# Kernel optimization log

Measured on AMD Instinct MI355X. Metric: run time of the kernel, lower is better.

The kernel has to match this reference:

```python
import jax, jax.numpy as jnp
import numpy as np

N = 10000      # nodes
E = 160000     # edges (before self-loops)
IN = 128       # input channels
H1, C1 = 8, 128   # layer-1 heads / per-head channels
OUT = 64       # output channels
NEG_SLOPE = 0.2   # PyG GATConv leaky_relu slope


def _glorot(key, shape):
    fan = shape[0] + shape[-1]
    return jax.random.normal(key, shape, jnp.float32) * np.float32(np.sqrt(2.0 / fan))


def setup_inputs() -> dict:
    key = jax.random.key(0)
    ks = jax.random.split(key, 10)
    x = jax.random.normal(ks[0], (N, IN), jnp.float32)
    edge_index = jax.random.randint(ks[1], (2, E), 0, N, dtype=jnp.int64)
    return {
        "x": x,
        "edge_index": edge_index,
        "W1": _glorot(ks[2], (IN, H1 * C1)),
        "a_src1": _glorot(ks[3], (H1, C1)),
        "a_dst1": _glorot(ks[4], (H1, C1)),
        "b1": jnp.zeros((H1 * C1,), jnp.float32),
        "W2": _glorot(ks[5], (H1 * C1, OUT)),
        "a_src2": _glorot(ks[6], (1, OUT)),
        "a_dst2": _glorot(ks[7], (1, OUT)),
        "b2": jnp.zeros((OUT,), jnp.float32),
    }


def gat_conv(x, src, dst, W, a_src, a_dst, bias, heads, ch, concat):
    n = x.shape[0]
    h = (x @ W).reshape(n, heads, ch)                 # [N,H,C]
    alpha_s = jnp.sum(h * a_src, axis=-1)             # [N,H]
    alpha_d = jnp.sum(h * a_dst, axis=-1)             # [N,H]
    e = jax.nn.leaky_relu(alpha_s[src] + alpha_d[dst], NEG_SLOPE)  # [E',H]
    # segment softmax over incoming edges of each dst node
    m = jax.ops.segment_max(e, dst, num_segments=n)
    e = jnp.exp(e - m[dst])
    s = jax.ops.segment_sum(e, dst, num_segments=n)
    alpha = e / (s[dst] + 1e-16)                      # [E',H]
    msg = h[src] * alpha[:, :, None]                  # [E',H,C]
    out = jax.ops.segment_sum(msg, dst, num_segments=n)  # [N,H,C]
    out = out.reshape(n, heads * ch) if concat else jnp.mean(out, axis=1)
    return out + bias


def reference(x, edge_index, W1, a_src1, a_dst1, b1, W2, a_src2, a_dst2, b2):
    n = x.shape[0]
    loops = jnp.arange(n, dtype=edge_index.dtype)     # PyG add_self_loops=True
    src = jnp.concatenate([edge_index[0], loops])
    dst = jnp.concatenate([edge_index[1], loops])
    h = jax.nn.elu(gat_conv(x, src, dst, W1, a_src1, a_dst1, b1, H1, C1, True))
    # dropout is identity in eval mode
    return gat_conv(h, src, dst, W2, a_src2, a_dst2, b2, 1, OUT, False)
```

## Files before the change

kernel.cpp:

```cpp
#include <hip/hip_runtime.h>
#include <math.h>


#define NEG_SLOPE 0.2f

typedef short bf16x8 __attribute__((ext_vector_type(8)));
typedef float f32x4 __attribute__((ext_vector_type(4)));

__device__ __forceinline__ float leaky(float v) { return v >= 0.0f ? v : NEG_SLOPE * v; }

__device__ __forceinline__ unsigned short f2bf(float f) {
    unsigned u = __float_as_uint(f);
    u += 0x7FFFu + ((u >> 16) & 1u);
    return (unsigned short)(u >> 16);
}


__global__ __launch_bounds__(256) void prep_count(
    const float* __restrict__ W1, const float* __restrict__ a_src1,
    const float* __restrict__ a_dst1, const float* __restrict__ W2,
    const int* __restrict__ ei,
    float* __restrict__ As_t, float* __restrict__ Ad_t,
    unsigned short* __restrict__ W1bT, unsigned short* __restrict__ W2bT,
    int* __restrict__ counts, int E, int N) {
    int b = blockIdx.x;
    __shared__ unsigned short tile[32][33];
    if (b < 4) {
        int i = b * 256 + threadIdx.x;
        int k = i >> 3, h = i & 7;
        float ss = 0.f, sd = 0.f;
        for (int c = 0; c < 128; c += 4) {
            float4 w = *(const float4*)(W1 + (size_t)k * 1024 + h * 128 + c);
            float4 a = *(const float4*)(a_src1 + h * 128 + c);
            float4 d = *(const float4*)(a_dst1 + h * 128 + c);
            ss += w.x * a.x + w.y * a.y + w.z * a.z + w.w * a.w;
            sd += w.x * d.x + w.y * d.y + w.z * d.z + w.w * d.w;
        }
        As_t[h * 132 + k] = ss;
        Ad_t[h * 132 + k] = sd;
    } else if (b < 132) {
        int bb = b - 4;
        int kt = bb & 3, hct = bb >> 2;
        int j = threadIdx.x & 31;
        int i0 = threadIdx.x >> 5;
        for (int i = i0; i < 32; i += 8)
            tile[i][j] = f2bf(W1[(size_t)(kt * 32 + i) * 1024 + hct * 32 + j]);
        __syncthreads();
        for (int i = i0; i < 32; i += 8) {
            int hc = hct * 32 + i, k = kt * 32 + j;
            int h = hc >> 7, c = hc & 127;
            W1bT[h * 16384 + c * 128 + k] = tile[j][i];
        }
    } else if (b < 196) {
        int bb = b - 132;
        int kt = bb & 31, ctile = bb >> 5;
        int j = threadIdx.x & 31;
        int i0 = threadIdx.x >> 5;
        for (int i = i0; i < 32; i += 8)
            tile[i][j] = f2bf(W2[(size_t)(kt * 32 + i) * 64 + ctile * 32 + j]);
        __syncthreads();
        for (int i = i0; i < 32; i += 8)
            W2bT[(size_t)(ctile * 32 + i) * 1024 + kt * 32 + j] = tile[j][i];
    } else {
        int i = (b - 196) * 256 + threadIdx.x;
        int M = E + N;
        if (i >= M) return;
        int dst = (i < E) ? ei[E + i] : (i - E);
        atomicAdd(&counts[dst], 1);
    }
}


__global__ __launch_bounds__(1024) void alpha_scan(
    const float* __restrict__ x, const float* __restrict__ As_t, const float* __restrict__ Ad_t,
    float* __restrict__ as1, float* __restrict__ ad1,
    const int* __restrict__ counts, int* __restrict__ offsets,
    int* __restrict__ cursor, int N, int nb_alpha) {
    int t = threadIdx.x;
    if ((int)blockIdx.x < nb_alpha) {
        __shared__ float sAs[1056], sAd[1056];
        for (int i = t; i < 1056; i += 1024) {
            sAs[i] = As_t[i];
            sAd[i] = Ad_t[i];
        }
        __syncthreads();
        int node = blockIdx.x * 128 + (t >> 3);
        int h = t & 7;
        if (node >= N) return;
        const float* sa = sAs + h * 132;
        const float* sd = sAd + h * 132;
        float accs = 0.f, accd = 0.f;
        for (int k = 0; k < 128; k += 4) {
            float4 xv = *(const float4*)(x + (size_t)node * 128 + k);
            float4 av = *(const float4*)(sa + k);
            float4 dv = *(const float4*)(sd + k);
            accs += xv.x * av.x + xv.y * av.y + xv.z * av.z + xv.w * av.w;
            accd += xv.x * dv.x + xv.y * dv.y + xv.z * dv.z + xv.w * dv.w;
        }
        as1[node * 8 + h] = accs;
        ad1[node * 8 + h] = accd;
    } else {
        __shared__ int wsum[16];
        int per = (N + 1023) / 1024;
        int base = t * per;
        int s = 0;
        for (int j = 0; j < per; j++) {
            int idx = base + j;
            if (idx < N) s += counts[idx];
        }
        int lane = t & 63, wid = t >> 6;
        int inc = s;
#pragma unroll
        for (int off = 1; off <= 32; off <<= 1) {
            int v = __shfl_up(inc, off);
            if (lane >= off) inc += v;
        }
        if (lane == 63) wsum[wid] = inc;
        __syncthreads();
        if (t < 16) {
            int v = wsum[t];
            int iv = v;
#pragma unroll
            for (int off = 1; off <= 8; off <<= 1) {
                int u = __shfl_up(iv, off);
                if (t >= off) iv += u;
            }
            wsum[t] = iv - v;
        }
        __syncthreads();
        int run = wsum[wid] + inc - s;
        for (int j = 0; j < per; j++) {
            int idx = base + j;
            if (idx < N) {
                offsets[idx] = run;
                cursor[idx] = run;
                run += counts[idx];
            }
        }
        if (t == 1023) offsets[N] = run;
    }
}


__global__ __launch_bounds__(256) void fill_w1(
    const int* __restrict__ ei, int* __restrict__ cursor,
    const float* __restrict__ as1, const float* __restrict__ ad1,
    int* __restrict__ srcs, float* __restrict__ wbuf, int E, int N) {
    int i = blockIdx.x * blockDim.x + threadIdx.x;
    int M = E + N;
    if (i >= M) return;
    int src, dst;
    if (i < E) { src = ei[i]; dst = ei[E + i]; }
    else       { src = dst = i - E; }
    int pos = atomicAdd(&cursor[dst], 1);
    srcs[pos] = src;
    float4 a0 = *(const float4*)(as1 + (size_t)src * 8);
    float4 a1 = *(const float4*)(as1 + (size_t)src * 8 + 4);
    float4 b0 = *(const float4*)(ad1 + (size_t)dst * 8);
    float4 b1 = *(const float4*)(ad1 + (size_t)dst * 8 + 4);
    float4 w0, w1;
    w0.x = __expf(leaky(a0.x + b0.x));
    w0.y = __expf(leaky(a0.y + b0.y));
    w0.z = __expf(leaky(a0.z + b0.z));
    w0.w = __expf(leaky(a0.w + b0.w));
    w1.x = __expf(leaky(a1.x + b1.x));
    w1.y = __expf(leaky(a1.y + b1.y));
    w1.z = __expf(leaky(a1.z + b1.z));
    w1.w = __expf(leaky(a1.w + b1.w));
    *(float4*)(wbuf + (size_t)pos * 8)     = w0;
    *(float4*)(wbuf + (size_t)pos * 8 + 4) = w1;
}


__global__ __launch_bounds__(256) void l1_gather(
    const float* __restrict__ x, const float* __restrict__ wbuf,
    const int* __restrict__ offsets, const int* __restrict__ srcs,
    unsigned short* __restrict__ y_b, int N) {
    int n = blockIdx.x * 4 + (threadIdx.x >> 6);
    if (n >= N) return;
    int lane = threadIdx.x & 63;
    int beg = offsets[n];
    int deg = offsets[n + 1] - beg;
    float2 acc[8];
#pragma unroll
    for (int h = 0; h < 8; h++) acc[h] = make_float2(0.f, 0.f);
    float4 ws0 = make_float4(0.f, 0.f, 0.f, 0.f);
    float4 ws1 = make_float4(0.f, 0.f, 0.f, 0.f);
    const float* xb = x + lane * 2;
#define L1G_BODY(I)                                                              \
    {                                                                            \
        int s_ = srcs[beg + (I)];                                                \
        float4 w0_ = *(const float4*)(wbuf + (size_t)(beg + (I)) * 8);           \
        float4 w1_ = *(const float4*)(wbuf + (size_t)(beg + (I)) * 8 + 4);       \
        float2 xv_ = *(const float2*)(xb + (size_t)s_ * 128);                    \
        ws0.x += w0_.x; ws0.y += w0_.y; ws0.z += w0_.z; ws0.w += w0_.w;          \
        ws1.x += w1_.x; ws1.y += w1_.y; ws1.z += w1_.z; ws1.w += w1_.w;          \
        acc[0].x = fmaf(w0_.x, xv_.x, acc[0].x); acc[0].y = fmaf(w0_.x, xv_.y, acc[0].y); \
        acc[1].x = fmaf(w0_.y, xv_.x, acc[1].x); acc[1].y = fmaf(w0_.y, xv_.y, acc[1].y); \
        acc[2].x = fmaf(w0_.z, xv_.x, acc[2].x); acc[2].y = fmaf(w0_.z, xv_.y, acc[2].y); \
        acc[3].x = fmaf(w0_.w, xv_.x, acc[3].x); acc[3].y = fmaf(w0_.w, xv_.y, acc[3].y); \
        acc[4].x = fmaf(w1_.x, xv_.x, acc[4].x); acc[4].y = fmaf(w1_.x, xv_.y, acc[4].y); \
        acc[5].x = fmaf(w1_.y, xv_.x, acc[5].x); acc[5].y = fmaf(w1_.y, xv_.y, acc[5].y); \
        acc[6].x = fmaf(w1_.z, xv_.x, acc[6].x); acc[6].y = fmaf(w1_.z, xv_.y, acc[6].y); \
        acc[7].x = fmaf(w1_.w, xv_.x, acc[7].x); acc[7].y = fmaf(w1_.w, xv_.y, acc[7].y); \
    }
    int i = 0;
    for (; i + 4 <= deg; i += 4) {
        L1G_BODY(i) L1G_BODY(i + 1) L1G_BODY(i + 2) L1G_BODY(i + 3)
    }
    for (; i < deg; i++) { L1G_BODY(i) }
#undef L1G_BODY
    float inv[8] = {1.f / (ws0.x + 1e-16f), 1.f / (ws0.y + 1e-16f),
                    1.f / (ws0.z + 1e-16f), 1.f / (ws0.w + 1e-16f),
                    1.f / (ws1.x + 1e-16f), 1.f / (ws1.y + 1e-16f),
                    1.f / (ws1.z + 1e-16f), 1.f / (ws1.w + 1e-16f)};
    unsigned short* dst = y_b + (size_t)n * 1024 + lane * 2;
#pragma unroll
    for (int h = 0; h < 8; h++) {
        unsigned lo = f2bf(acc[h].x * inv[h]);
        unsigned hi = f2bf(acc[h].y * inv[h]);
        *(unsigned*)(dst + h * 128) = lo | (hi << 16);
    }
}


__global__ __launch_bounds__(512) void l12_gemm(
    const unsigned short* __restrict__ y_b, const unsigned short* __restrict__ W1bT,
    const float* __restrict__ b1, const unsigned short* __restrict__ W2bT,
    const float* __restrict__ a_src2, const float* __restrict__ a_dst2,
    float* __restrict__ h2, float* __restrict__ as2, float* __restrict__ ad2, int N) {
    int nb = blockIdx.x * 16;
    int w = threadIdx.x >> 6;
    int lane = threadIdx.x & 63;
    int n16 = lane & 15, quad = lane >> 4;
    __shared__ unsigned short hb[16 * 1032];
    __shared__ float red[4][64][4];
    __shared__ float sA[4][16], sD[4][16];
    int node_a = nb + n16;
    const unsigned short* ya = y_b + (size_t)(node_a < N ? node_a : 0) * 1024
                             + w * 128 + quad * 8;
    bf16x8 af[4];
#pragma unroll
    for (int ks = 0; ks < 4; ks++) af[ks] = *(const bf16x8*)(ya + ks * 32);
#pragma unroll
    for (int cti = 0; cti < 8; cti++) {
        int cc = cti * 16;
        const unsigned short* Wh = W1bT + w * 16384 + (size_t)(cc + n16) * 128 + quad * 8;
        f32x4 acc = (f32x4){0.f, 0.f, 0.f, 0.f};
#pragma unroll
        for (int ks = 0; ks < 4; ks++) {
            bf16x8 b = *(const bf16x8*)(Wh + ks * 32);
            acc = __builtin_amdgcn_mfma_f32_16x16x32_bf16(af[ks], b, acc, 0, 0, 0);
        }
        int c = w * 128 + cc + n16;
        float bias = b1[c];
#pragma unroll
        for (int r = 0; r < 4; r++) {
            float v = acc[r] + bias;
            v = v > 0.f ? v : expm1f(v);
            hb[(quad * 4 + r) * 1032 + c] = f2bf(v);
        }
    }
    __syncthreads();
    int ct2 = w & 3, kh = w >> 2;
    const unsigned short* arow = hb + n16 * 1032 + kh * 512 + quad * 8;
    const unsigned short* brow = W2bT + (size_t)(ct2 * 16 + n16) * 1024 + kh * 512 + quad * 8;
    f32x4 acc = (f32x4){0.f, 0.f, 0.f, 0.f};
#pragma unroll
    for (int ks = 0; ks < 16; ks++) {
        bf16x8 a = *(const bf16x8*)(arow + ks * 32);
        bf16x8 b = *(const bf16x8*)(brow + ks * 32);
        acc = __builtin_amdgcn_mfma_f32_16x16x32_bf16(a, b, acc, 0, 0, 0);
    }
    if (kh == 1) {
#pragma unroll
        for (int r = 0; r < 4; r++) red[ct2][lane][r] = acc[r];
    }
    __syncthreads();
    if (kh == 0) {
#pragma unroll
        for (int r = 0; r < 4; r++) acc[r] += red[ct2][lane][r];
        int c2 = ct2 * 16 + n16;
        float asc = a_src2[c2], adc = a_dst2[c2];
        float pav[4], pdv[4];
#pragma unroll
        for (int r = 0; r < 4; r++) {
            int node = nb + quad * 4 + r;
            if (node < N) h2[(size_t)node * 64 + c2] = acc[r];
            pav[r] = acc[r] * asc;
            pdv[r] = acc[r] * adc;
#pragma unroll
            for (int mm = 1; mm <= 8; mm <<= 1) {
                pav[r] += __shfl_xor(pav[r], mm);
                pdv[r] += __shfl_xor(pdv[r], mm);
            }
        }
        if (n16 == 0) {
#pragma unroll
            for (int r = 0; r < 4; r++) {
                sA[ct2][quad * 4 + r] = pav[r];
                sD[ct2][quad * 4 + r] = pdv[r];
            }
        }
    }
    __syncthreads();
    if (threadIdx.x < 16) {
        int node = nb + threadIdx.x;
        if (node < N) {
            as2[node] = sA[0][threadIdx.x] + sA[1][threadIdx.x] + sA[2][threadIdx.x] + sA[3][threadIdx.x];
            ad2[node] = sD[0][threadIdx.x] + sD[1][threadIdx.x] + sD[2][threadIdx.x] + sD[3][threadIdx.x];
        }
    }
}


__global__ __launch_bounds__(256) void l2_gather(
    const float* __restrict__ h2, const float* __restrict__ as2,
    const float* __restrict__ ad2, const float* __restrict__ b2,
    const int* __restrict__ offsets, const int* __restrict__ srcs,
    float* __restrict__ out, int N) {
    int n = blockIdx.x * 4 + (threadIdx.x >> 6);
    if (n >= N) return;
    int lane = threadIdx.x & 63;
    int beg = offsets[n];
    int deg = offsets[n + 1] - beg;
    float adn = ad2[n];
    float acc = 0.f, wsum = 0.f;
    int i = 0;
    for (; i + 4 <= deg; i += 4) {
        int s0 = srcs[beg + i],     s1 = srcs[beg + i + 1];
        int s2 = srcs[beg + i + 2], s3 = srcs[beg + i + 3];
        float w0 = __expf(leaky(as2[s0] + adn));
        float w1 = __expf(leaky(as2[s1] + adn));
        float w2 = __expf(leaky(as2[s2] + adn));
        float w3 = __expf(leaky(as2[s3] + adn));
        float v0 = h2[(size_t)s0 * 64 + lane];
        float v1 = h2[(size_t)s1 * 64 + lane];
        float v2 = h2[(size_t)s2 * 64 + lane];
        float v3 = h2[(size_t)s3 * 64 + lane];
        wsum += w0 + w1 + w2 + w3;
        acc = fmaf(w0, v0, acc);
        acc = fmaf(w1, v1, acc);
        acc = fmaf(w2, v2, acc);
        acc = fmaf(w3, v3, acc);
    }
    for (; i < deg; i++) {
        int s = srcs[beg + i];
        float w = __expf(leaky(as2[s] + adn));
        wsum += w;
        acc = fmaf(w, h2[(size_t)s * 64 + lane], acc);
    }
    out[(size_t)n * 64 + lane] = acc / (wsum + 1e-16f) + b2[lane];
}


static inline size_t align_up(size_t v, size_t a) { return (v + a - 1) / a * a; }

extern "C" void kernel_launch(void* const* d_in, const int* in_sizes, int n_in,
                              void* d_out, int out_size, void* d_ws, size_t ws_size,
                              hipStream_t stream) {
    const float* x      = (const float*)d_in[0];
    const int*   ei     = (const int*)d_in[1];
    const float* W1     = (const float*)d_in[2];
    const float* a_src1 = (const float*)d_in[3];
    const float* a_dst1 = (const float*)d_in[4];
    const float* b1     = (const float*)d_in[5];
    const float* W2     = (const float*)d_in[6];
    const float* a_src2 = (const float*)d_in[7];
    const float* a_dst2 = (const float*)d_in[8];
    const float* b2     = (const float*)d_in[9];
    float* out = (float*)d_out;

    int N = in_sizes[0] / 128;
    int E = in_sizes[1] / 2;
    int M = E + N;

    char* p = (char*)d_ws;
    size_t off = 0;
    auto carve = [&](size_t bytes) {
        void* r = p + off;
        off = align_up(off + bytes, 256);
        return r;
    };
    int*            counts  = (int*)carve((size_t)N * 4);
    int*            offsets = (int*)carve((size_t)(N + 1) * 4);
    int*            cursor  = (int*)carve((size_t)N * 4);
    int*            srcs    = (int*)carve((size_t)M * 4);
    float*          As_t    = (float*)carve(1056 * 4);
    float*          Ad_t    = (float*)carve(1056 * 4);
    float*          as1     = (float*)carve((size_t)N * 8 * 4);
    float*          ad1     = (float*)carve((size_t)N * 8 * 4);
    float*          as2     = (float*)carve((size_t)N * 4);
    float*          ad2     = (float*)carve((size_t)N * 4);
    float*          h2      = (float*)carve((size_t)N * 64 * 4);
    float*          wbuf    = (float*)carve((size_t)M * 8 * 4);
    unsigned short* W1bT    = (unsigned short*)carve((size_t)8 * 128 * 128 * 2);
    unsigned short* W2bT    = (unsigned short*)carve((size_t)64 * 1024 * 2);
    unsigned short* y_b     = (unsigned short*)carve((size_t)N * 1024 * 2);
    (void)ws_size;

    int nb_count = (M + 255) / 256;
    int nb_alpha = (N + 127) / 128;

    hipMemsetAsync(counts, 0, (size_t)N * 4, stream);
    prep_count<<<196 + nb_count, 256, 0, stream>>>(W1, a_src1, a_dst1, W2, ei,
                                                   As_t, Ad_t, W1bT, W2bT, counts, E, N);
    alpha_scan<<<nb_alpha + 1, 1024, 0, stream>>>(x, As_t, Ad_t, as1, ad1,
                                                  counts, offsets, cursor, N, nb_alpha);
    fill_w1<<<nb_count, 256, 0, stream>>>(ei, cursor, as1, ad1, srcs, wbuf, E, N);
    l1_gather<<<(N + 3) / 4, 256, 0, stream>>>(x, wbuf, offsets, srcs, y_b, N);
    l12_gemm<<<(N + 15) / 16, 512, 0, stream>>>(y_b, W1bT, b1, W2bT, a_src2, a_dst2,
                                                h2, as2, ad2, N);
    l2_gather<<<(N + 3) / 4, 256, 0, stream>>>(h2, as2, ad2, b2, offsets, srcs, out, N);
}
```

Measured before the change: 195.9 us.

## Fuse layer-1 neighbor aggregation into the layer-1/2 GEMM kernel

Removes the separate l1_gather kernel and its bf16 N×1024 y_b intermediate. Each lane of the GEMM kernel now aggregates, for its node and head, weighted x rows over the incoming edges directly into registers before the MFMA. This saves one launch and a round trip of about 20 MB through global memory. In exchange, each thread walks a whole edge list serially with 32 accumulators, so register pressure rises and load balance across the 16 nodes in a block may be poor. Each x row is also re-read once per head instead of once per node.

Result: slower. 316.5 us (+61.6%).

```diff
diff --git a/kernel.cpp b/kernel.cpp
--- a/kernel.cpp
+++ b/kernel.cpp
@@ -172,61 +172,11 @@
 }
 
 
-__global__ __launch_bounds__(256) void l1_gather(
+__global__ __launch_bounds__(512) void l12_gemm(
     const float* __restrict__ x, const float* __restrict__ wbuf,
     const int* __restrict__ offsets, const int* __restrict__ srcs,
-    unsigned short* __restrict__ y_b, int N) {
-    int n = blockIdx.x * 4 + (threadIdx.x >> 6);
-    if (n >= N) return;
-    int lane = threadIdx.x & 63;
-    int beg = offsets[n];
-    int deg = offsets[n + 1] - beg;
-    float2 acc[8];
-#pragma unroll
-    for (int h = 0; h < 8; h++) acc[h] = make_float2(0.f, 0.f);
-    float4 ws0 = make_float4(0.f, 0.f, 0.f, 0.f);
-    float4 ws1 = make_float4(0.f, 0.f, 0.f, 0.f);
-    const float* xb = x + lane * 2;
-#define L1G_BODY(I)                                                              \
-    {                                                                            \
-        int s_ = srcs[beg + (I)];                                                \
-        float4 w0_ = *(const float4*)(wbuf + (size_t)(beg + (I)) * 8);           \
-        float4 w1_ = *(const float4*)(wbuf + (size_t)(beg + (I)) * 8 + 4);       \
-        float2 xv_ = *(const float2*)(xb + (size_t)s_ * 128);                    \
-        ws0.x += w0_.x; ws0.y += w0_.y; ws0.z += w0_.z; ws0.w += w0_.w;          \
-        ws1.x += w1_.x; ws1.y += w1_.y; ws1.z += w1_.z; ws1.w += w1_.w;          \
-        acc[0].x = fmaf(w0_.x, xv_.x, acc[0].x); acc[0].y = fmaf(w0_.x, xv_.y, acc[0].y); \
-        acc[1].x = fmaf(w0_.y, xv_.x, acc[1].x); acc[1].y = fmaf(w0_.y, xv_.y, acc[1].y); \
-        acc[2].x = fmaf(w0_.z, xv_.x, acc[2].x); acc[2].y = fmaf(w0_.z, xv_.y, acc[2].y); \
-        acc[3].x = fmaf(w0_.w, xv_.x, acc[3].x); acc[3].y = fmaf(w0_.w, xv_.y, acc[3].y); \
-        acc[4].x = fmaf(w1_.x, xv_.x, acc[4].x); acc[4].y = fmaf(w1_.x, xv_.y, acc[4].y); \
-        acc[5].x = fmaf(w1_.y, xv_.x, acc[5].x); acc[5].y = fmaf(w1_.y, xv_.y, acc[5].y); \
-        acc[6].x = fmaf(w1_.z, xv_.x, acc[6].x); acc[6].y = fmaf(w1_.z, xv_.y, acc[6].y); \
-        acc[7].x = fmaf(w1_.w, xv_.x, acc[7].x); acc[7].y = fmaf(w1_.w, xv_.y, acc[7].y); \
-    }
-    int i = 0;
-    for (; i + 4 <= deg; i += 4) {
-        L1G_BODY(i) L1G_BODY(i + 1) L1G_BODY(i + 2) L1G_BODY(i + 3)
-    }
-    for (; i < deg; i++) { L1G_BODY(i) }
-#undef L1G_BODY
-    float inv[8] = {1.f / (ws0.x + 1e-16f), 1.f / (ws0.y + 1e-16f),
-                    1.f / (ws0.z + 1e-16f), 1.f / (ws0.w + 1e-16f),
-                    1.f / (ws1.x + 1e-16f), 1.f / (ws1.y + 1e-16f),
-                    1.f / (ws1.z + 1e-16f), 1.f / (ws1.w + 1e-16f)};
-    unsigned short* dst = y_b + (size_t)n * 1024 + lane * 2;
-#pragma unroll
-    for (int h = 0; h < 8; h++) {
-        unsigned lo = f2bf(acc[h].x * inv[h]);
-        unsigned hi = f2bf(acc[h].y * inv[h]);
-        *(unsigned*)(dst + h * 128) = lo | (hi << 16);
-    }
-}
-
-
-__global__ __launch_bounds__(512) void l12_gemm(
-    const unsigned short* __restrict__ y_b, const unsigned short* __restrict__ W1bT,
-    const float* __restrict__ b1, const unsigned short* __restrict__ W2bT,
+    const unsigned short* __restrict__ W1bT, const float* __restrict__ b1,
+    const unsigned short* __restrict__ W2bT,
     const float* __restrict__ a_src2, const float* __restrict__ a_dst2,
     float* __restrict__ h2, float* __restrict__ as2, float* __restrict__ ad2, int N) {
     int nb = blockIdx.x * 16;
@@ -236,12 +186,48 @@
     __shared__ unsigned short hb[16 * 1032];
     __shared__ float red[4][64][4];
     __shared__ float sA[4][16], sD[4][16];
-    int node_a = nb + n16;
-    const unsigned short* ya = y_b + (size_t)(node_a < N ? node_a : 0) * 1024
-                             + w * 128 + quad * 8;
+    int node = nb + n16;
+    bool vn = node < N;
+    int beg = vn ? offsets[node] : 0;
+    int deg = vn ? (offsets[node + 1] - beg) : 0;
+    float a0[32];
+#pragma unroll
+    for (int q = 0; q < 32; q++) a0[q] = 0.f;
+    float wsum = 0.f;
+    const float* xq = x + quad * 8;
+#define P0_BODY(I)                                                           \
+    {                                                                        \
+        int s_ = srcs[beg + (I)];                                            \
+        float we_ = wbuf[(size_t)(beg + (I)) * 8 + w];                       \
+        wsum += we_;                                                         \
+        const float* xr_ = xq + (size_t)s_ * 128;                            \
+        _Pragma("unroll")                                                    \
+        for (int ks = 0; ks < 4; ks++) {                                     \
+            float4 v0_ = *(const float4*)(xr_ + ks * 32);                    \
+            float4 v1_ = *(const float4*)(xr_ + ks * 32 + 4);                \
+            a0[ks * 8 + 0] = fmaf(we_, v0_.x, a0[ks * 8 + 0]);               \
+            a0[ks * 8 + 1] = fmaf(we_, v0_.y, a0[ks * 8 + 1]);               \
+            a0[ks * 8 + 2] = fmaf(we_, v0_.z, a0[ks * 8 + 2]);               \
+            a0[ks * 8 + 3] = fmaf(we_, v0_.w, a0[ks * 8 + 3]);               \
+            a0[ks * 8 + 4] = fmaf(we_, v1_.x, a0[ks * 8 + 4]);               \
+            a0[ks * 8 + 5] = fmaf(we_, v1_.y, a0[ks * 8 + 5]);               \
+            a0[ks * 8 + 6] = fmaf(we_, v1_.z, a0[ks * 8 + 6]);               \
+            a0[ks * 8 + 7] = fmaf(we_, v1_.w, a0[ks * 8 + 7]);               \
+        }                                                                    \
+    }
+    int i = 0;
+    for (; i + 2 <= deg; i += 2) { P0_BODY(i) P0_BODY(i + 1) }
+    for (; i < deg; i++) { P0_BODY(i) }
+#undef P0_BODY
+    float inv = 1.0f / (wsum + 1e-16f);
     bf16x8 af[4];
 #pragma unroll
-    for (int ks = 0; ks < 4; ks++) af[ks] = *(const bf16x8*)(ya + ks * 32);
+    for (int ks = 0; ks < 4; ks++) {
+        union { bf16x8 v; unsigned short u[8]; } tmp;
+#pragma unroll
+        for (int j = 0; j < 8; j++) tmp.u[j] = f2bf(a0[ks * 8 + j] * inv);
+        af[ks] = tmp.v;
+    }
 #pragma unroll
     for (int cti = 0; cti < 8; cti++) {
         int cc = cti * 16;
@@ -285,8 +271,8 @@
         float pav[4], pdv[4];
 #pragma unroll
         for (int r = 0; r < 4; r++) {
-            int node = nb + quad * 4 + r;
-            if (node < N) h2[(size_t)node * 64 + c2] = acc[r];
+            int nd = nb + quad * 4 + r;
+            if (nd < N) h2[(size_t)nd * 64 + c2] = acc[r];
             pav[r] = acc[r] * asc;
             pdv[r] = acc[r] * adc;
 #pragma unroll
@@ -305,10 +291,10 @@
     }
     __syncthreads();
     if (threadIdx.x < 16) {
-        int node = nb + threadIdx.x;
-        if (node < N) {
-            as2[node] = sA[0][threadIdx.x] + sA[1][threadIdx.x] + sA[2][threadIdx.x] + sA[3][threadIdx.x];
-            ad2[node] = sD[0][threadIdx.x] + sD[1][threadIdx.x] + sD[2][threadIdx.x] + sD[3][threadIdx.x];
+        int nd = nb + threadIdx.x;
+        if (nd < N) {
+            as2[nd] = sA[0][threadIdx.x] + sA[1][threadIdx.x] + sA[2][threadIdx.x] + sA[3][threadIdx.x];
+            ad2[nd] = sD[0][threadIdx.x] + sD[1][threadIdx.x] + sD[2][threadIdx.x] + sD[3][threadIdx.x];
         }
     }
 }
@@ -396,7 +382,6 @@
     float*          wbuf    = (float*)carve((size_t)M * 8 * 4);
     unsigned short* W1bT    = (unsigned short*)carve((size_t)8 * 128 * 128 * 2);
     unsigned short* W2bT    = (unsigned short*)carve((size_t)64 * 1024 * 2);
-    unsigned short* y_b     = (unsigned short*)carve((size_t)N * 1024 * 2);
     (void)ws_size;
 
     int nb_count = (M + 255) / 256;
@@ -408,8 +393,8 @@
     alpha_scan<<<nb_alpha + 1, 1024, 0, stream>>>(x, As_t, Ad_t, as1, ad1,
                                                   counts, offsets, cursor, N, nb_alpha);
     fill_w1<<<nb_count, 256, 0, stream>>>(ei, cursor, as1, ad1, srcs, wbuf, E, N);
-    l1_gather<<<(N + 3) / 4, 256, 0, stream>>>(x, wbuf, offsets, srcs, y_b, N);
-    l12_gemm<<<(N + 15) / 16, 512, 0, stream>>>(y_b, W1bT, b1, W2bT, a_src2, a_dst2,
+    l12_gemm<<<(N + 15) / 16, 512, 0, stream>>>(x, wbuf, offsets, srcs,
+                                                W1bT, b1, W2bT, a_src2, a_dst2,
                                                 h2, as2, ad2, N);
     l2_gather<<<(N + 3) / 4, 256, 0, stream>>>(h2, as2, ad2, b2, offsets, srcs, out, N);
 }
```
